# Optimization experiments

Measured on AMD Instinct MI355X. Metric: run time of the kernel, lower is better.

Reference implementation:

```python
import jax, jax.numpy as jnp
import numpy as np

B, T, D = 4, 1024, 768
HW = 32            # H = W = sqrt(T)
DS = D // 16       # d_state = 48
CHUNK = 8          # items_each_chunk (must divide W)


def _ln(x, w, b, eps=1e-5):
    mu = x.mean(-1, keepdims=True)
    var = ((x - mu) ** 2).mean(-1, keepdims=True)
    return (x - mu) / jnp.sqrt(var + eps) * w + b


def _conv1x1(x, w):  # x: (B,C,H,W), w: (O,C)
    return jnp.einsum('bchw,oc->bohw', x, w)


def _dwconv(x, w, b, pad):  # depthwise conv, w: (C,1,k,k)
    y = jax.lax.conv_general_dilated(
        x, w, (1, 1), [(pad, pad), (pad, pad)],
        dimension_numbers=('NCHW', 'OIHW', 'NCHW'),
        feature_group_count=x.shape[1])
    if b is not None:
        y = y + b[None, :, None, None]
    return y


def _norm_gates(Gl, Gm, Gr):
    gl, gm, gr = jax.nn.sigmoid(Gl), jax.nn.sigmoid(Gm), jax.nn.sigmoid(Gr)
    s = gl + gm + gr
    s = s.at[:, :, 0, :].set(gm[:, :, 0, :] + gr[:, :, 0, :])    # top row: no h-1 neighbor
    s = s.at[:, :, -1, :].set(gl[:, :, -1, :] + gm[:, :, -1, :])  # bottom row: no h+1 neighbor
    s = jnp.maximum(s, 1e-7)
    return gl / s, gm / s, gr / s


def _gspn_scan(X, L, Gl, Gm, Gr, chunk):
    # GateRecurrent2dnoind: scan along W in independent chunks of `chunk` columns.
    # H[:, :, h, t] = L*X + Gl*Hprev[h-1] + Gm*Hprev[h] + Gr*Hprev[h+1], Hprev=0 at chunk start.
    b, c, h, w = X.shape
    nc = w // chunk

    def to_scan(a):  # (B,C,H,W) -> (chunk, B, C, H, nc)
        return a.reshape(b, c, h, nc, chunk).transpose(4, 0, 1, 2, 3)

    xs, ls, gls, gms, grs = map(to_scan, (X, L, Gl, Gm, Gr))

    def step(hprev, inp):
        x, l, gl, gm, gr = inp
        h_up = jnp.pad(hprev[:, :, :-1], ((0, 0), (0, 0), (1, 0), (0, 0)))
        h_dn = jnp.pad(hprev[:, :, 1:], ((0, 0), (0, 0), (0, 1), (0, 0)))
        hn = l * x + gl * h_up + gm * hprev + gr * h_dn
        return hn, hn

    _, ys = jax.lax.scan(step, jnp.zeros((b, c, h, nc), X.dtype), (xs, ls, gls, gms, grs))
    return ys.transpose(1, 2, 3, 4, 0).reshape(b, c, h, w)


def setup_inputs() -> dict:
    key = jax.random.key(0)
    ks = jax.random.split(key, 16)
    s = 0.02
    return {
        'hidden_states': jax.random.normal(ks[0], (B, T, D), jnp.float32),
        'norm_w': jnp.ones((D,), jnp.float32),
        'norm_b': jnp.zeros((D,), jnp.float32),
        'in_proj_w': jax.random.normal(ks[1], (D, D), jnp.float32) * s,
        'conv7_w': jax.random.normal(ks[2], (D, 1, 7, 7), jnp.float32) * s,
        'conv7_b': jnp.zeros((D,), jnp.float32),
        'xdown_w': jax.random.normal(ks[3], (DS, D), jnp.float32) * s,
        'wup_w': jax.random.normal(ks[4], (12 * D, DS), jnp.float32) * s,
        'lup_w': jax.random.normal(ks[5], (4 * D, DS), jnp.float32) * s,
        'uup_w': jax.random.normal(ks[6], (4 * D, DS), jnp.float32) * s,
        'dcoef_w': jax.random.normal(ks[7], (4 * D, DS), jnp.float32) * s,
        'm_w': jax.random.normal(ks[8], (4,), jnp.float32) * 0.25,
        'outconv_w': jax.random.normal(ks[9], (D, D), jnp.float32) * s,
        'outdconv_w': jax.random.normal(ks[10], (D, 1, 3, 3), jnp.float32) * s,
        'outproj_w': jax.random.normal(ks[11], (D, D), jnp.float32) * s,
    }


def reference(hidden_states, norm_w, norm_b, in_proj_w, conv7_w, conv7_b,
              xdown_w, wup_w, lup_w, uup_w, dcoef_w, m_w,
              outconv_w, outdconv_w, outproj_w):
    b, t, d = hidden_states.shape
    hh = ww = HW
    shortcut = hidden_states
    x = _ln(shortcut, norm_w, norm_b)                      # (B,T,D)
    x = x.transpose(0, 2, 1).reshape(b, d, hh, ww)         # (B,D,H,W)
    x = _conv1x1(x, in_proj_w)
    x = _dwconv(x, conv7_w, conv7_b, 3)
    xp = _conv1x1(x, xdown_w)                              # (B,ds,H,W)
    ws = _conv1x1(xp, wup_w)                               # (B,12D,H,W)
    Ls = _conv1x1(xp, lup_w)                               # (B,4D,H,W)
    Us = _conv1x1(xp, uup_w)
    Ds = _conv1x1(xp, dcoef_w)
    # 4 scan directions: [x, x^T, flip_w(x), flip_w(x^T)]
    x_hwwh = jnp.stack([x, x.transpose(0, 1, 3, 2)], axis=1)       # (B,2,D,H,W)
    xs = jnp.concatenate([x_hwwh, x_hwwh[..., ::-1]], axis=1)      # (B,4,D,H,W)
    xs = xs.reshape(b, 4 * d, hh, ww)
    Gl, Gm, Gr = ws[:, :4 * d], ws[:, 4 * d:8 * d], ws[:, 8 * d:]
    gl, gm, gr = _norm_gates(Gl, Gm, Gr)
    out = _gspn_scan(xs, Ls, gl, gm, gr, CHUNK)
    out = out * Us + xs * Ds
    out = out.reshape(b, 4, d, hh, ww)
    out = jnp.einsum('bkdhw,k->bdhw', out, m_w)            # m_conv (1x1 over 4 dirs)
    out = _conv1x1(out, outconv_w)
    out = _dwconv(out, outdconv_w, None, 1)
    out = out * jax.nn.relu(out)
    out = out.reshape(b, d, t).transpose(0, 2, 1)
    out = out @ outproj_w.T
    return out, shortcut
```

## Files before the change

### kernel.cpp

```cpp
#include <hip/hip_runtime.h>

typedef unsigned short u16;
typedef unsigned int u32;
typedef __attribute__((ext_vector_type(8))) short short8v;
typedef __attribute__((ext_vector_type(4))) float f32x4;
typedef __attribute__((ext_vector_type(2))) unsigned u32x2v;

#define DD 768
#define PP 1024
#define NTOK 4096

__device__ __forceinline__ u16 f2bf(float f) {
  u32 u = __builtin_bit_cast(u32, f);
  u += 0x7fffu + ((u >> 16) & 1u);
  return (u16)(u >> 16);
}
__device__ __forceinline__ float b2f(u16 v) {
  return __builtin_bit_cast(float, (u32)v << 16);
}
__device__ __forceinline__ u32 pk_trunc(float fa, float fb) {
  return __builtin_amdgcn_perm(__builtin_bit_cast(u32, fa), __builtin_bit_cast(u32, fb), 0x07060302u);
}
__device__ __forceinline__ float ex8(const short8v& v, int j) {
  const u32 dw = ((const u32*)&v)[j >> 1];
  return __builtin_bit_cast(float, (j & 1) ? (dw & 0xffff0000u) : (dw << 16));
}
__device__ __forceinline__ float dpp_shr1(float x) {
  return __builtin_bit_cast(float,
      __builtin_amdgcn_update_dpp(0, __builtin_bit_cast(int, x), 0x138, 0xf, 0xf, true));
}
__device__ __forceinline__ float dpp_shl1(float x) {
  return __builtin_bit_cast(float,
      __builtin_amdgcn_update_dpp(0, __builtin_bit_cast(int, x), 0x130, 0xf, 0xf, true));
}
__device__ __forceinline__ float xhalf_sum(float p) {
#if __has_builtin(__builtin_amdgcn_permlane32_swap)
  u32x2v sw = __builtin_amdgcn_permlane32_swap(__builtin_bit_cast(u32, p),
                                               __builtin_bit_cast(u32, p), false, false);
  return __builtin_bit_cast(float, sw[0]) + __builtin_bit_cast(float, sw[1]);
#else
  return p + __shfl_xor(p, 32, 64);
#endif
}

__global__ __launch_bounds__(256) void prep_ln_k(const float* __restrict__ hs,
                                                 const float* __restrict__ gw, const float* __restrict__ gb,
                                                 u16* __restrict__ lnout, float* __restrict__ shortcut,
                                                 const float* __restrict__ win, u16* __restrict__ wInB,
                                                 const float* __restrict__ wout, u16* __restrict__ wOutB,
                                                 const float* __restrict__ wprj, u16* __restrict__ wPrjB,
                                                 const float* __restrict__ xdw, u16* __restrict__ wXdB,
                                                 const float* __restrict__ wup, const float* __restrict__ lup,
                                                 const float* __restrict__ uup, const float* __restrict__ dco,
                                                 u16* __restrict__ wB) {
  const int id = blockIdx.x;
  const int t = threadIdx.x;
  if (id < 4096) {
    const int tok = id;
    const float* xr = hs + (size_t)tok * DD;
    float v0 = xr[t], v1 = xr[t + 256], v2 = xr[t + 512];
    float s = v0 + v1 + v2;
    float q = v0 * v0 + v1 * v1 + v2 * v2;
#pragma unroll
    for (int off = 32; off > 0; off >>= 1) {
      s += __shfl_down(s, off, 64);
      q += __shfl_down(q, off, 64);
    }
    __shared__ float ss[4], qs[4];
    const int wid = t >> 6, lane = t & 63;
    if (lane == 0) { ss[wid] = s; qs[wid] = q; }
    __syncthreads();
    const float st = ss[0] + ss[1] + ss[2] + ss[3];
    const float qt = qs[0] + qs[1] + qs[2] + qs[3];
    const float mu = st * (1.f / 768.f);
    const float var = qt * (1.f / 768.f) - mu * mu;
    const float rstd = rsqrtf(var + 1e-5f);
    float* sc = shortcut + (size_t)tok * DD;
    u16* lo = lnout + (size_t)tok * DD;
    sc[t] = v0; sc[t + 256] = v1; sc[t + 512] = v2;
    lo[t]       = f2bf((v0 - mu) * rstd * gw[t] + gb[t]);
    lo[t + 256] = f2bf((v1 - mu) * rstd * gw[t + 256] + gb[t + 256]);
    lo[t + 512] = f2bf((v2 - mu) * rstd * gw[t + 512] + gb[t + 512]);
    return;
  }
  const int id2 = id - 4096;
  if (id2 < 6912) {
    const int m = id2 / 2304;
    const int i = (id2 - m * 2304) * 256 + t;
    const float* s = (m == 0) ? win : (m == 1) ? wout : wprj;
    u16* d = (m == 0) ? wInB : (m == 1) ? wOutB : wPrjB;
    d[i] = f2bf(s[i]);
  } else if (id2 < 7104) {
    const int i = (id2 - 6912) * 256 + t;
    const int r = i / DD;
    wXdB[i] = (r < 48) ? f2bf(xdw[i]) : (u16)0;
  } else {
    const int c = id2 - 7104;
    u16* dst = wB + (size_t)c * 2048;
    for (int i = t; i < 2048; i += 256) {
      const int row = i >> 6, s = i & 63;
      u16 v = 0;
      if (row < 24 && s < 48) {
        const int k = row & 3, type = row >> 2;
        const int ch = k * DD + c;
        const float* src;
        if (type < 3) src = wup + ((size_t)(type * 3072 + ch)) * 48;
        else if (type == 3) src = lup + (size_t)ch * 48;
        else if (type == 4) src = uup + (size_t)ch * 48;
        else src = dco + (size_t)ch * 48;
        v = f2bf(src[s]);
      }
      dst[i] = v;
    }
  }
}

template <int BSRC>
__global__ __launch_bounds__(256) void gemm_bf16(const u16* __restrict__ A,
                                                 const u16* __restrict__ Bt,
                                                 void* __restrict__ outv, const int mode) {
  __shared__ u16 Al[64][72];
  __shared__ u16 BlF[144 * 72];
  const int t = threadIdx.x;
  const int ntile = blockIdx.x * 128;
  const int mtile = blockIdx.y * 64;
  const int bb = ntile >> 10, pq0 = ntile & 1023;
  const int wid = t >> 6, lane = t & 63;
  const int m0 = (wid & 1) * 32, n0 = (wid >> 1) * 64;
  const int l15 = lane & 15, quad = lane >> 4;
  f32x4 acc[2][4];
#pragma unroll
  for (int mi = 0; mi < 2; ++mi)
#pragma unroll
    for (int ni = 0; ni < 4; ++ni) acc[mi][ni] = (f32x4){0.f, 0.f, 0.f, 0.f};
  const int ra = t >> 2, sa = t & 3;
  const u16* ag = A + (size_t)(mtile + ra) * DD + sa * 16;
  const int rb = t >> 1, hb = t & 1;
  const u16* bg = Bt + (size_t)(ntile + rb) * DD + hb * 32;
  const int chp = t >> 4, tok0 = (t & 15) * 8;
  const u16* bgc0 = Bt + ((size_t)(bb * DD + chp * 2)) * PP + pq0 + tok0;
  const u16* bgc1 = Bt + ((size_t)(bb * DD + (chp + 16) * 2)) * PP + pq0 + tok0;
  uint4 pa0, pa1, pb0, pb1, pb2, pb3;
#define LOADK(k0)                                                              \
  {                                                                            \
    pa0 = *reinterpret_cast<const uint4*>(ag + (k0));                          \
    pa1 = *reinterpret_cast<const uint4*>(ag + (k0) + 8);                      \
    if (BSRC == 0) {                                                           \
      pb0 = *reinterpret_cast<const uint4*>(bg + (k0));                        \
      pb1 = *reinterpret_cast<const uint4*>(bg + (k0) + 8);                    \
      pb2 = *reinterpret_cast<const uint4*>(bg + (k0) + 16);                   \
      pb3 = *reinterpret_cast<const uint4*>(bg + (k0) + 24);                   \
    } else {                                                                   \
      pb0 = *reinterpret_cast<const uint4*>(bgc0 + (size_t)(k0) * PP);         \
      pb1 = *reinterpret_cast<const uint4*>(bgc0 + (size_t)((k0) + 1) * PP);   \
      pb2 = *reinterpret_cast<const uint4*>(bgc1 + (size_t)(k0) * PP);         \
      pb3 = *reinterpret_cast<const uint4*>(bgc1 + (size_t)((k0) + 1) * PP);   \
    }                                                                          \
  }
  LOADK(0);
  for (int k0 = 0; k0 < DD; k0 += 64) {
    __syncthreads();
    *reinterpret_cast<uint4*>(&Al[ra][sa * 16]) = pa0;
    *reinterpret_cast<uint4*>(&Al[ra][sa * 16 + 8]) = pa1;
    if (BSRC == 0) {
      const int pr = rb + (rb >> 3);
      *reinterpret_cast<uint4*>(&BlF[pr * 72 + hb * 32]) = pb0;
      *reinterpret_cast<uint4*>(&BlF[pr * 72 + hb * 32 + 8]) = pb1;
      *reinterpret_cast<uint4*>(&BlF[pr * 72 + hb * 32 + 16]) = pb2;
      *reinterpret_cast<uint4*>(&BlF[pr * 72 + hb * 32 + 24]) = pb3;
    } else {
      union { uint4 v; u16 u[8]; } ua, ub, uc, ud;
      ua.v = pb0; ub.v = pb1; uc.v = pb2; ud.v = pb3;
#pragma unroll
      for (int i2 = 0; i2 < 8; ++i2) {
        const int prow = (tok0 + i2 + ((tok0 + i2) >> 3)) * 72;
        *reinterpret_cast<u32*>(&BlF[prow + chp * 2]) =
            (u32)ua.u[i2] | ((u32)ub.u[i2] << 16);
        *reinterpret_cast<u32*>(&BlF[prow + chp * 2 + 32]) =
            (u32)uc.u[i2] | ((u32)ud.u[i2] << 16);
      }
    }
    __syncthreads();
    if (k0 + 64 < DD) LOADK(k0 + 64);
    short8v af[2][2], bfr[4][2];
#pragma unroll
    for (int mi = 0; mi < 2; ++mi)
#pragma unroll
      for (int ks = 0; ks < 2; ++ks)
        af[mi][ks] = *reinterpret_cast<const short8v*>(&Al[m0 + mi * 16 + l15][ks * 32 + quad * 8]);
#pragma unroll
    for (int ni = 0; ni < 4; ++ni) {
      const int tl = n0 + ni * 16 + l15;
      const int prow = (tl + (tl >> 3)) * 72;
#pragma unroll
      for (int ks = 0; ks < 2; ++ks)
        bfr[ni][ks] = *reinterpret_cast<const short8v*>(&BlF[prow + ks * 32 + quad * 8]);
    }
#pragma unroll
    for (int mi = 0; mi < 2; ++mi)
#pragma unroll
      for (int ni = 0; ni < 4; ++ni) {
        acc[mi][ni] = __builtin_amdgcn_mfma_f32_16x16x32_bf16(af[mi][0], bfr[ni][0], acc[mi][ni], 0, 0, 0);
        acc[mi][ni] = __builtin_amdgcn_mfma_f32_16x16x32_bf16(af[mi][1], bfr[ni][1], acc[mi][ni], 0, 0, 0);
      }
  }
#undef LOADK
#pragma unroll
  for (int mi = 0; mi < 2; ++mi) {
#pragma unroll
    for (int ni = 0; ni < 4; ++ni) {
      const int ob = mtile + m0 + mi * 16 + quad * 4;
      const int pg = ntile + n0 + ni * 16 + l15;
      if (mode == 1) {
        *reinterpret_cast<f32x4*>((float*)outv + (size_t)pg * DD + ob) = acc[mi][ni];
      } else {
        const int pq = pg & 1023;
        u16* dstb = (u16*)outv;
#pragma unroll
        for (int r = 0; r < 4; ++r)
          dstb[((size_t)(bb * DD + ob + r)) * PP + pq] = f2bf(acc[mi][ni][r]);
      }
    }
  }
}

__global__ __launch_bounds__(256) void xdgemm_k(const u16* __restrict__ A,
                                                const u16* __restrict__ Ycm,
                                                u16* __restrict__ xpA) {
  __shared__ u16 Al[64][72];
  __shared__ u16 Bl[16][72];
  const int t = threadIdx.x;
  const int ntile = blockIdx.x * 16;
  const int bb = ntile >> 10, pq0 = ntile & 1023;
  const int wid = t >> 6, lane = t & 63, l15 = lane & 15, quad = lane >> 4;
  f32x4 acc = (f32x4){0.f, 0.f, 0.f, 0.f};
  const int arow = t >> 2, aks = (t & 3) * 16;
  const u16* ag = A + (size_t)arow * DD + aks;
  const int chp = t >> 3;
  const int tk0 = (t & 7) * 2;
  const u16* bg0 = Ycm + ((size_t)(bb * DD + chp * 2)) * PP + pq0 + tk0;
  for (int k0 = 0; k0 < DD; k0 += 64) {
    const uint4 a0 = *reinterpret_cast<const uint4*>(ag + k0);
    const uint4 a1 = *reinterpret_cast<const uint4*>(ag + k0 + 8);
    const u32 b0 = *reinterpret_cast<const u32*>(bg0 + (size_t)k0 * PP);
    const u32 b1 = *reinterpret_cast<const u32*>(bg0 + (size_t)(k0 + 1) * PP);
    __syncthreads();
    *reinterpret_cast<uint4*>(&Al[arow][aks]) = a0;
    *reinterpret_cast<uint4*>(&Al[arow][aks + 8]) = a1;
    *reinterpret_cast<u32*>(&Bl[tk0][chp * 2]) = (b0 & 0xffffu) | (b1 << 16);
    *reinterpret_cast<u32*>(&Bl[tk0 + 1][chp * 2]) = (b0 >> 16) | (b1 & 0xffff0000u);
    __syncthreads();
#pragma unroll
    for (int ks = 0; ks < 2; ++ks) {
      const short8v af = *reinterpret_cast<const short8v*>(&Al[wid * 16 + l15][ks * 32 + quad * 8]);
      const short8v bf = *reinterpret_cast<const short8v*>(&Bl[l15][ks * 32 + quad * 8]);
      acc = __builtin_amdgcn_mfma_f32_16x16x32_bf16(af, bf, acc, 0, 0, 0);
    }
  }
  const int pq = pq0 + l15;
  const int i = ((pq & 31) >> 4) * 512 + (pq >> 5) * 16 + (pq & 15);
  u16* dst = xpA + ((size_t)(bb * 1024 + i)) * 64 + wid * 16 + quad * 4;
  *reinterpret_cast<uint2*>(dst) = make_uint2(pk_trunc(acc[1], acc[0]), pk_trunc(acc[3], acc[2]));
}

__global__ __launch_bounds__(256) void dwconv7_k(const u16* __restrict__ x,
                                                 const float* __restrict__ wgt,
                                                 const float* __restrict__ bias,
                                                 u16* __restrict__ y) {
  const int bc = blockIdx.x;
  const int c = bc % DD;
  __shared__ float tile[38 * 38];
  __shared__ float wl[49];
  __shared__ float bsh[1];
  const int t = threadIdx.x;
  for (int i = t; i < 38 * 38; i += 256) tile[i] = 0.f;
  __syncthreads();
  const u16* xr = x + (size_t)bc * PP;
  for (int i = t; i < 512; i += 256) {
    const u32 v = reinterpret_cast<const u32*>(xr)[i];
    const int p0 = i * 2;
    const int h = p0 >> 5, w = p0 & 31;
    tile[(h + 3) * 38 + w + 3] = b2f((u16)v);
    tile[(h + 3) * 38 + w + 4] = b2f((u16)(v >> 16));
  }
  if (t < 49) wl[t] = wgt[c * 49 + t];
  if (t == 0) bsh[0] = bias[c];
  __syncthreads();
  u16* yo = y + (size_t)bc * PP;
  const int w = t & 31, hb = t >> 5;
  const float bv = bsh[0];
  float a0 = bv, a1 = bv, a2 = bv, a3 = bv;
#pragma unroll
  for (int rr = 0; rr < 10; ++rr) {
    float row[7];
#pragma unroll
    for (int kw = 0; kw < 7; ++kw) row[kw] = tile[(hb * 4 + rr) * 38 + w + kw];
    if (rr < 7) {
#pragma unroll
      for (int kw = 0; kw < 7; ++kw) a0 = fmaf(wl[rr * 7 + kw], row[kw], a0);
    }
    if (rr >= 1 && rr < 8) {
#pragma unroll
      for (int kw = 0; kw < 7; ++kw) a1 = fmaf(wl[(rr - 1) * 7 + kw], row[kw], a1);
    }
    if (rr >= 2 && rr < 9) {
#pragma unroll
      for (int kw = 0; kw < 7; ++kw) a2 = fmaf(wl[(rr - 2) * 7 + kw], row[kw], a2);
    }
    if (rr >= 3) {
#pragma unroll
      for (int kw = 0; kw < 7; ++kw) a3 = fmaf(wl[(rr - 3) * 7 + kw], row[kw], a3);
    }
  }
  yo[(hb * 4 + 0) * 32 + w] = f2bf(a0);
  yo[(hb * 4 + 1) * 32 + w] = f2bf(a1);
  yo[(hb * 4 + 2) * 32 + w] = f2bf(a2);
  yo[(hb * 4 + 3) * 32 + w] = f2bf(a3);
}

__global__ __launch_bounds__(256) void dwconv3_k(const u16* __restrict__ x,
                                                 const float* __restrict__ wgt,
                                                 u16* __restrict__ y) {
  const int bc = blockIdx.x;
  const int c = bc % DD;
  __shared__ float tile[34 * 34];
  __shared__ float wl[9];
  const int t = threadIdx.x;
  for (int i = t; i < 34 * 34; i += 256) tile[i] = 0.f;
  __syncthreads();
  const u16* xr = x + (size_t)bc * PP;
  for (int i = t; i < 512; i += 256) {
    const u32 v = reinterpret_cast<const u32*>(xr)[i];
    const int p0 = i * 2;
    const int h = p0 >> 5, w = p0 & 31;
    tile[(h + 1) * 34 + w + 1] = b2f((u16)v);
    tile[(h + 1) * 34 + w + 2] = b2f((u16)(v >> 16));
  }
  if (t < 9) wl[t] = wgt[c * 9 + t];
  __syncthreads();
  u16* yo = y + (size_t)bc * PP;
  const int w = t & 31, hb = t >> 5;
  float a0 = 0.f, a1 = 0.f, a2 = 0.f, a3 = 0.f;
#pragma unroll
  for (int rr = 0; rr < 6; ++rr) {
    float row[3];
#pragma unroll
    for (int kw = 0; kw < 3; ++kw) row[kw] = tile[(hb * 4 + rr) * 34 + w + kw];
    if (rr < 3) {
#pragma unroll
      for (int kw = 0; kw < 3; ++kw) a0 = fmaf(wl[rr * 3 + kw], row[kw], a0);
    }
    if (rr >= 1 && rr < 4) {
#pragma unroll
      for (int kw = 0; kw < 3; ++kw) a1 = fmaf(wl[(rr - 1) * 3 + kw], row[kw], a1);
    }
    if (rr >= 2 && rr < 5) {
#pragma unroll
      for (int kw = 0; kw < 3; ++kw) a2 = fmaf(wl[(rr - 2) * 3 + kw], row[kw], a2);
    }
    if (rr >= 3) {
#pragma unroll
      for (int kw = 0; kw < 3; ++kw) a3 = fmaf(wl[(rr - 3) * 3 + kw], row[kw], a3);
    }
  }
  const float r0 = a0 > 0.f ? a0 * a0 : 0.f;
  const float r1 = a1 > 0.f ? a1 * a1 : 0.f;
  const float r2 = a2 > 0.f ? a2 * a2 : 0.f;
  const float r3 = a3 > 0.f ? a3 * a3 : 0.f;
  yo[(hb * 4 + 0) * 32 + w] = f2bf(r0);
  yo[(hb * 4 + 1) * 32 + w] = f2bf(r1);
  yo[(hb * 4 + 2) * 32 + w] = f2bf(r2);
  yo[(hb * 4 + 3) * 32 + w] = f2bf(r3);
}

#define ACT_SWZ(row, col) ((col) ^ (((((col) >> 6) ^ (row)) & 7) << 3))
#define PSWZ(r) ((((r) ^ ((r) >> 3)) & 3) << 3)

__device__ __forceinline__ void produce_half(u16* __restrict__ actbuf,
                                             const u16* __restrict__ ab,
                                             const short8v bw[2][2],
                                             int l15, int quad, int g) {
#pragma unroll
  for (int mt = 0; mt < 8; ++mt) {
    const u16* ar = ab + (mt * 16 + l15) * 64 + quad * 8;
    const short8v a0 = *reinterpret_cast<const short8v*>(ar);
    const short8v a1 = *reinterpret_cast<const short8v*>(ar + 32);
    f32x4 acc0 = {0.f, 0.f, 0.f, 0.f}, acc1 = {0.f, 0.f, 0.f, 0.f};
    acc0 = __builtin_amdgcn_mfma_f32_16x16x32_bf16(a0, bw[0][0], acc0, 0, 0, 0);
    acc0 = __builtin_amdgcn_mfma_f32_16x16x32_bf16(a1, bw[0][1], acc0, 0, 0, 0);
    acc1 = __builtin_amdgcn_mfma_f32_16x16x32_bf16(a0, bw[1][0], acc1, 0, 0, 0);
    acc1 = __builtin_amdgcn_mfma_f32_16x16x32_bf16(a1, bw[1][1], acc1, 0, 0, 0);
    const int qb = g * 128 + mt * 16 + quad * 4;
    const int cs = ACT_SWZ(l15, qb);
    *reinterpret_cast<uint2*>(&actbuf[l15 * 512 + cs]) =
        make_uint2(pk_trunc(acc0[1], acc0[0]), pk_trunc(acc0[3], acc0[2]));
    if (l15 < 8)
      *reinterpret_cast<uint2*>(&actbuf[(16 + l15) * 512 + cs]) =
          make_uint2(pk_trunc(acc1[1], acc1[0]), pk_trunc(acc1[3], acc1[2]));
  }
}

__device__ __forceinline__ void consume_half(const u16* __restrict__ actbuf,
                                             const u16* __restrict__ planeTc,
                                             const u16* __restrict__ y2row,
                                             u16* __restrict__ outpc,
                                             float mw, int dpair, int cs2, int d, int h, int half) {
  __builtin_amdgcn_s_setprio(1);
  const int k = dpair * 2 + d;
  const int hc = half * 2 + cs2;
  const int colb = h * 16 + cs2 * 8;
  const int wst = dpair ? (24 - hc * 8) : (hc * 8);
  short8v vPr;
  if (d == 0) vPr = *reinterpret_cast<const short8v*>(y2row + h * 32 + wst);
  else        vPr = *reinterpret_cast<const short8v*>(planeTc + h * 40 + (wst ^ PSWZ(h)));
  short8v vPe;
  {
    const u32* s = (const u32*)&vPr;
    u32* dq = (u32*)&vPe;
    if (dpair) {
      dq[0] = (s[3] >> 16) | (s[3] << 16);
      dq[1] = (s[2] >> 16) | (s[2] << 16);
      dq[2] = (s[1] >> 16) | (s[1] << 16);
      dq[3] = (s[0] >> 16) | (s[0] << 16);
    } else {
      dq[0] = s[0]; dq[1] = s[1]; dq[2] = s[2]; dq[3] = s[3];
    }
  }
#define ACTP(row) (*reinterpret_cast<const short8v*>(&actbuf[(row) * 512 + ACT_SWZ((row), colb)]))
  const short8v vGl = ACTP(0 + k);
  const short8v vGm = ACTP(4 + k);
  const short8v vGr = ACTP(8 + k);
  const short8v vL  = ACTP(12 + k);
  const short8v vU  = ACTP(16 + k);
  const short8v vD  = ACTP(20 + k);
#undef ACTP
  const bool top = (h == 0), bot = (h == 31);
  float H = 0.f, prev = 0.f;
  u32 ox[4];
#pragma unroll
  for (int j = 0; j < 8; ++j) {
    float el = __expf(-ex8(vGl, j));
    const float em = __expf(-ex8(vGm, j));
    float er = __expf(-ex8(vGr, j));
    if (top) el = 1e30f;
    if (bot) er = 1e30f;
    const float pl2 = 1.f + el, pm = 1.f + em, pr = 1.f + er;
    const float ul = pm * pr, um = pl2 * pr, ur = pl2 * pm;
    const float rcpS = __builtin_amdgcn_rcpf(ul + um + ur);
    const float xv = ex8(vPe, j);
    const float Lx = ex8(vL, j) * xv;
    const float up = dpp_shr1(H);
    const float dn = dpp_shl1(H);
    H = fmaf(ul * rcpS, up, fmaf(um * rcpS, H, fmaf(ur * rcpS, dn, Lx)));
    float part = fmaf(H, ex8(vU, j), xv * ex8(vD, j)) * mw;
    part = xhalf_sum(part);
    if (j & 1) ox[j >> 1] = pk_trunc(part, prev);
    else prev = part;
  }
  if (d == 0) {
    uint4 o;
    o.x = ox[0]; o.y = ox[1]; o.z = ox[2]; o.w = ox[3];
    *reinterpret_cast<uint4*>(&outpc[h * 64 + dpair * 32 + ((hc * 8) ^ ((h & 3) << 3))]) = o;
  }
  __builtin_amdgcn_s_setprio(0);
}

__global__ __launch_bounds__(512, 4) void scan_k(const u16* __restrict__ y2b,
                                                 const u16* __restrict__ xpA,
                                                 const u16* __restrict__ wB,
                                                 const float* __restrict__ mwp,
                                                 u16* __restrict__ out1) {
  const int bc2 = blockIdx.x;
  const int b = bc2 / 384;
  const int cpair = bc2 - b * 384;
  const int c0 = cpair * 2;
  __shared__ __align__(16) u16 actA[24 * 512];
  __shared__ __align__(16) u16 actB[24 * 512];
  __shared__ __align__(16) u16 planeT[2][1280];
  __shared__ __align__(16) u16 outp[2][32 * 64];
  const int t = threadIdx.x;
  const int wid = t >> 6, lane = t & 63, l15 = lane & 15, quad = lane >> 4;
  const int ch = wid >> 2;
  const int g = wid & 3;
  const int dpair = g & 1, cs2 = g >> 1;
  const int d = lane >> 5, h = lane & 31;
  const int c = c0 + ch;
  const int bc = b * DD + c;
  {
    const int pch = t >> 8, idx = t & 255;
    const u16* yp = y2b + (size_t)(b * DD + c0 + pch) * PP;
#pragma unroll
    for (int i2 = 0; i2 < 2; ++i2) {
      const int i = idx + i2 * 256;
      const u32 v = reinterpret_cast<const u32*>(yp)[i];
      const int p0 = i * 2;
      const int hh = p0 >> 5, ww = p0 & 31;
      planeT[pch][ww * 40 + (hh ^ PSWZ(ww))] = (u16)v;
      planeT[pch][(ww + 1) * 40 + (hh ^ PSWZ(ww + 1))] = (u16)(v >> 16);
    }
  }
  const u16* wc = wB + (size_t)c * 2048;
  short8v bw[2][2];
#pragma unroll
  for (int nt = 0; nt < 2; ++nt)
#pragma unroll
    for (int ks = 0; ks < 2; ++ks)
      bw[nt][ks] = *reinterpret_cast<const short8v*>(wc + (nt * 16 + l15) * 64 + ks * 32 + quad * 8);
  const u16* xb = xpA + ((size_t)(b * 1024)) * 64;
  const u16* y2row = y2b + (size_t)bc * PP;
  const float mw = mwp[dpair * 2 + d];
  if (ch == 0) produce_half(actA, xb + (size_t)(g * 128) * 64, bw, l15, quad, g);
  __syncthreads();
  if (ch == 0) consume_half(actA, planeT[0], y2row, outp[0], mw, dpair, cs2, d, h, 0);
  else         produce_half(actB, xb + (size_t)(g * 128) * 64, bw, l15, quad, g);
  __syncthreads();
  if (ch == 1) consume_half(actB, planeT[1], y2row, outp[1], mw, dpair, cs2, d, h, 0);
  else         produce_half(actA, xb + (size_t)(512 + g * 128) * 64, bw, l15, quad, g);
  __syncthreads();
  if (ch == 0) consume_half(actA, planeT[0], y2row, outp[0], mw, dpair, cs2, d, h, 1);
  else         produce_half(actB, xb + (size_t)(512 + g * 128) * 64, bw, l15, quad, g);
  __syncthreads();
  if (ch == 1) consume_half(actB, planeT[1], y2row, outp[1], mw, dpair, cs2, d, h, 1);
  __syncthreads();
  const int hh2 = t >> 4, wp = t & 15;
  const int wsw = (wp * 2) ^ ((hh2 & 3) << 3);
#pragma unroll
  for (int cc = 0; cc < 2; ++cc) {
    const u32 u0 = *reinterpret_cast<const u32*>(&outp[cc][hh2 * 64 + wsw]);
    const u32 u1 = *reinterpret_cast<const u32*>(&outp[cc][hh2 * 64 + 32 + wsw]);
    const float v0 = b2f((u16)u0) + b2f((u16)u1);
    const float v1 = b2f((u16)(u0 >> 16)) + b2f((u16)(u1 >> 16));
    *reinterpret_cast<u32*>(out1 + (size_t)(b * DD + c0 + cc) * PP + hh2 * 32 + wp * 2) =
        pk_trunc(v1, v0);
  }
}

extern "C" void kernel_launch(void* const* d_in, const int* in_sizes, int n_in,
                              void* d_out, int out_size, void* d_ws, size_t ws_size,
                              hipStream_t stream) {
  const float* hs   = (const float*)d_in[0];
  const float* nw   = (const float*)d_in[1];
  const float* nb   = (const float*)d_in[2];
  const float* win  = (const float*)d_in[3];
  const float* c7w  = (const float*)d_in[4];
  const float* c7b  = (const float*)d_in[5];
  const float* xdw  = (const float*)d_in[6];
  const float* wupw = (const float*)d_in[7];
  const float* lupw = (const float*)d_in[8];
  const float* uupw = (const float*)d_in[9];
  const float* dcow = (const float*)d_in[10];
  const float* mww  = (const float*)d_in[11];
  const float* wout = (const float*)d_in[12];
  const float* odw  = (const float*)d_in[13];
  const float* wprj = (const float*)d_in[14];
  float* out0 = (float*)d_out;
  float* shortcut = out0 + (size_t)NTOK * DD;

  char* ws = (char*)d_ws;
  u16* lnA    = (u16*)(ws + 0);
  u16* wInB   = (u16*)(ws + 6291456);
  u16* wOutB  = (u16*)(ws + 7471104);
  u16* wPrjB  = (u16*)(ws + 8650752);
  u16* wB     = (u16*)(ws + 9830400);
  u16* wXdB   = (u16*)(ws + 12976128);
  u16* xpA    = (u16*)(ws + 13074432);
  u16* y1b    = (u16*)(ws + 13598720);
  u16* y2b    = (u16*)(ws + 19890176);
  u16* out1   = (u16*)(ws + 26181632);
  u16* y3b    = y1b;
  u16* y4b    = out1;

  prep_ln_k<<<11968, 256, 0, stream>>>(hs, nw, nb, lnA, shortcut,
                                       win, wInB, wout, wOutB, wprj, wPrjB,
                                       xdw, wXdB, wupw, lupw, uupw, dcow, wB);
  gemm_bf16<0><<<dim3(32, 12), 256, 0, stream>>>(wInB, lnA, y1b, 3);
  dwconv7_k<<<3072, 256, 0, stream>>>(y1b, c7w, c7b, y2b);
  xdgemm_k<<<256, 256, 0, stream>>>(wXdB, y2b, xpA);
  scan_k<<<1536, 512, 0, stream>>>(y2b, xpA, wB, mww, out1);
  gemm_bf16<1><<<dim3(32, 12), 256, 0, stream>>>(wOutB, out1, y3b, 3);
  dwconv3_k<<<3072, 256, 0, stream>>>(y3b, odw, y4b);
  gemm_bf16<1><<<dim3(32, 12), 256, 0, stream>>>(wPrjB, y4b, out0, 1);
}
```

Measured before the change: 226.5 us.

## Load GEMM operands directly into MFMA registers, bypassing shared memory

Replaces the templated shared-memory GEMM with two kernels. The first (in_proj) loads A and B fragments straight from global memory into MFMA register layout, with no LDS and no barriers, and double-buffers the even and odd k-halves. The second (out_conv/out_proj) still transposes B through LDS, but now packs four channels per 8-byte store and loads A fragments directly from global memory. The aim is to cut LDS traffic and synchronisation, at the cost of less coalesced global loads and more reliance on cache for operand reuse.

```diff
diff --git a/kernel.cpp b/kernel.cpp
--- a/kernel.cpp
+++ b/kernel.cpp
@@ -115,11 +115,92 @@
   }
 }
 
-template <int BSRC>
-__global__ __launch_bounds__(256) void gemm_bf16(const u16* __restrict__ A,
-                                                 const u16* __restrict__ Bt,
-                                                 void* __restrict__ outv, const int mode) {
-  __shared__ u16 Al[64][72];
+__global__ __launch_bounds__(256) void gemm_nl(const u16* __restrict__ A,
+                                               const u16* __restrict__ Bt,
+                                               void* __restrict__ outv, const int mode) {
+  const int t = threadIdx.x;
+  const int ntile = blockIdx.x * 128;
+  const int mtile = blockIdx.y * 64;
+  const int bb = ntile >> 10;
+  const int wid = t >> 6, lane = t & 63;
+  const int m0 = (wid & 1) * 32, n0 = (wid >> 1) * 64;
+  const int l15 = lane & 15, quad = lane >> 4;
+  f32x4 acc[2][4];
+#pragma unroll
+  for (int mi = 0; mi < 2; ++mi)
+#pragma unroll
+    for (int ni = 0; ni < 4; ++ni) acc[mi][ni] = (f32x4){0.f, 0.f, 0.f, 0.f};
+  const u16* a0p = A + (size_t)(mtile + m0 + l15) * DD + quad * 8;
+  const u16* a1p = a0p + (size_t)16 * DD;
+  const u16* b0p = Bt + (size_t)(ntile + n0 + l15) * DD + quad * 8;
+  const u16* b1p = b0p + (size_t)16 * DD;
+  const u16* b2p = b0p + (size_t)32 * DD;
+  const u16* b3p = b0p + (size_t)48 * DD;
+  short8v a0e, a1e, b0e, b1e, b2e, b3e;
+  short8v a0o, a1o, b0o, b1o, b2o, b3o;
+#define LOADE(k0)                                              \
+  {                                                            \
+    a0e = *reinterpret_cast<const short8v*>(a0p + (k0));       \
+    a1e = *reinterpret_cast<const short8v*>(a1p + (k0));       \
+    b0e = *reinterpret_cast<const short8v*>(b0p + (k0));       \
+    b1e = *reinterpret_cast<const short8v*>(b1p + (k0));       \
+    b2e = *reinterpret_cast<const short8v*>(b2p + (k0));       \
+    b3e = *reinterpret_cast<const short8v*>(b3p + (k0));       \
+  }
+#define LOADO(k0)                                              \
+  {                                                            \
+    a0o = *reinterpret_cast<const short8v*>(a0p + (k0));       \
+    a1o = *reinterpret_cast<const short8v*>(a1p + (k0));       \
+    b0o = *reinterpret_cast<const short8v*>(b0p + (k0));       \
+    b1o = *reinterpret_cast<const short8v*>(b1p + (k0));       \
+    b2o = *reinterpret_cast<const short8v*>(b2p + (k0));       \
+    b3o = *reinterpret_cast<const short8v*>(b3p + (k0));       \
+  }
+  LOADE(0);
+  for (int k0 = 0; k0 < DD; k0 += 64) {
+    LOADO(k0 + 32);
+    acc[0][0] = __builtin_amdgcn_mfma_f32_16x16x32_bf16(a0e, b0e, acc[0][0], 0, 0, 0);
+    acc[0][1] = __builtin_amdgcn_mfma_f32_16x16x32_bf16(a0e, b1e, acc[0][1], 0, 0, 0);
+    acc[0][2] = __builtin_amdgcn_mfma_f32_16x16x32_bf16(a0e, b2e, acc[0][2], 0, 0, 0);
+    acc[0][3] = __builtin_amdgcn_mfma_f32_16x16x32_bf16(a0e, b3e, acc[0][3], 0, 0, 0);
+    acc[1][0] = __builtin_amdgcn_mfma_f32_16x16x32_bf16(a1e, b0e, acc[1][0], 0, 0, 0);
+    acc[1][1] = __builtin_amdgcn_mfma_f32_16x16x32_bf16(a1e, b1e, acc[1][1], 0, 0, 0);
+    acc[1][2] = __builtin_amdgcn_mfma_f32_16x16x32_bf16(a1e, b2e, acc[1][2], 0, 0, 0);
+    acc[1][3] = __builtin_amdgcn_mfma_f32_16x16x32_bf16(a1e, b3e, acc[1][3], 0, 0, 0);
+    if (k0 + 64 < DD) LOADE(k0 + 64);
+    acc[0][0] = __builtin_amdgcn_mfma_f32_16x16x32_bf16(a0o, b0o, acc[0][0], 0, 0, 0);
+    acc[0][1] = __builtin_amdgcn_mfma_f32_16x16x32_bf16(a0o, b1o, acc[0][1], 0, 0, 0);
+    acc[0][2] = __builtin_amdgcn_mfma_f32_16x16x32_bf16(a0o, b2o, acc[0][2], 0, 0, 0);
+    acc[0][3] = __builtin_amdgcn_mfma_f32_16x16x32_bf16(a0o, b3o, acc[0][3], 0, 0, 0);
+    acc[1][0] = __builtin_amdgcn_mfma_f32_16x16x32_bf16(a1o, b0o, acc[1][0], 0, 0, 0);
+    acc[1][1] = __builtin_amdgcn_mfma_f32_16x16x32_bf16(a1o, b1o, acc[1][1], 0, 0, 0);
+    acc[1][2] = __builtin_amdgcn_mfma_f32_16x16x32_bf16(a1o, b2o, acc[1][2], 0, 0, 0);
+    acc[1][3] = __builtin_amdgcn_mfma_f32_16x16x32_bf16(a1o, b3o, acc[1][3], 0, 0, 0);
+  }
+#undef LOADE
+#undef LOADO
+#pragma unroll
+  for (int mi = 0; mi < 2; ++mi) {
+#pragma unroll
+    for (int ni = 0; ni < 4; ++ni) {
+      const int ob = mtile + m0 + mi * 16 + quad * 4;
+      const int pg = ntile + n0 + ni * 16 + l15;
+      if (mode == 1) {
+        *reinterpret_cast<f32x4*>((float*)outv + (size_t)pg * DD + ob) = acc[mi][ni];
+      } else {
+        const int pq = pg & 1023;
+        u16* dstb = (u16*)outv;
+#pragma unroll
+        for (int r = 0; r < 4; ++r)
+          dstb[((size_t)(bb * DD + ob + r)) * PP + pq] = f2bf(acc[mi][ni][r]);
+      }
+    }
+  }
+}
+
+__global__ __launch_bounds__(256) void gemm_cm(const u16* __restrict__ A,
+                                               const u16* __restrict__ Bt,
+                                               void* __restrict__ outv, const int mode) {
   __shared__ u16 BlF[144 * 72];
   const int t = threadIdx.x;
   const int ntile = blockIdx.x * 128;
@@ -133,61 +214,50 @@
   for (int mi = 0; mi < 2; ++mi)
 #pragma unroll
     for (int ni = 0; ni < 4; ++ni) acc[mi][ni] = (f32x4){0.f, 0.f, 0.f, 0.f};
-  const int ra = t >> 2, sa = t & 3;
-  const u16* ag = A + (size_t)(mtile + ra) * DD + sa * 16;
-  const int rb = t >> 1, hb = t & 1;
-  const u16* bg = Bt + (size_t)(ntile + rb) * DD + hb * 32;
   const int chp = t >> 4, tok0 = (t & 15) * 8;
-  const u16* bgc0 = Bt + ((size_t)(bb * DD + chp * 2)) * PP + pq0 + tok0;
-  const u16* bgc1 = Bt + ((size_t)(bb * DD + (chp + 16) * 2)) * PP + pq0 + tok0;
-  uint4 pa0, pa1, pb0, pb1, pb2, pb3;
-#define LOADK(k0)                                                              \
-  {                                                                            \
-    pa0 = *reinterpret_cast<const uint4*>(ag + (k0));                          \
-    pa1 = *reinterpret_cast<const uint4*>(ag + (k0) + 8);                      \
-    if (BSRC == 0) {                                                           \
-      pb0 = *reinterpret_cast<const uint4*>(bg + (k0));                        \
-      pb1 = *reinterpret_cast<const uint4*>(bg + (k0) + 8);                    \
-      pb2 = *reinterpret_cast<const uint4*>(bg + (k0) + 16);                   \
-      pb3 = *reinterpret_cast<const uint4*>(bg + (k0) + 24);                   \
-    } else {                                                                   \
-      pb0 = *reinterpret_cast<const uint4*>(bgc0 + (size_t)(k0) * PP);         \
-      pb1 = *reinterpret_cast<const uint4*>(bgc0 + (size_t)((k0) + 1) * PP);   \
-      pb2 = *reinterpret_cast<const uint4*>(bgc1 + (size_t)(k0) * PP);         \
-      pb3 = *reinterpret_cast<const uint4*>(bgc1 + (size_t)((k0) + 1) * PP);   \
-    }                                                                          \
-  }
-  LOADK(0);
+  const u16* bgc = Bt + ((size_t)(bb * DD + chp * 4)) * PP + pq0 + tok0;
+  const u16* a0p = A + (size_t)(mtile + m0 + l15) * DD + quad * 8;
+  const u16* a1p = a0p + (size_t)16 * DD;
+  uint4 pb0, pb1, pb2, pb3;
+  short8v paf[2][2];
+#define LOADB(k0)                                                            \
+  {                                                                          \
+    pb0 = *reinterpret_cast<const uint4*>(bgc + (size_t)(k0) * PP);          \
+    pb1 = *reinterpret_cast<const uint4*>(bgc + (size_t)((k0) + 1) * PP);    \
+    pb2 = *reinterpret_cast<const uint4*>(bgc + (size_t)((k0) + 2) * PP);    \
+    pb3 = *reinterpret_cast<const uint4*>(bgc + (size_t)((k0) + 3) * PP);    \
+  }
+#define LOADA(k0)                                                            \
+  {                                                                          \
+    paf[0][0] = *reinterpret_cast<const short8v*>(a0p + (k0));               \
+    paf[0][1] = *reinterpret_cast<const short8v*>(a0p + (k0) + 32);          \
+    paf[1][0] = *reinterpret_cast<const short8v*>(a1p + (k0));               \
+    paf[1][1] = *reinterpret_cast<const short8v*>(a1p + (k0) + 32);          \
+  }
+  LOADB(0);
+  LOADA(0);
   for (int k0 = 0; k0 < DD; k0 += 64) {
     __syncthreads();
-    *reinterpret_cast<uint4*>(&Al[ra][sa * 16]) = pa0;
-    *reinterpret_cast<uint4*>(&Al[ra][sa * 16 + 8]) = pa1;
-    if (BSRC == 0) {
-      const int pr = rb + (rb >> 3);
-      *reinterpret_cast<uint4*>(&BlF[pr * 72 + hb * 32]) = pb0;
-      *reinterpret_cast<uint4*>(&BlF[pr * 72 + hb * 32 + 8]) = pb1;
-      *reinterpret_cast<uint4*>(&BlF[pr * 72 + hb * 32 + 16]) = pb2;
-      *reinterpret_cast<uint4*>(&BlF[pr * 72 + hb * 32 + 24]) = pb3;
-    } else {
+    {
       union { uint4 v; u16 u[8]; } ua, ub, uc, ud;
       ua.v = pb0; ub.v = pb1; uc.v = pb2; ud.v = pb3;
 #pragma unroll
       for (int i2 = 0; i2 < 8; ++i2) {
-        const int prow = (tok0 + i2 + ((tok0 + i2) >> 3)) * 72;
-        *reinterpret_cast<u32*>(&BlF[prow + chp * 2]) =
-            (u32)ua.u[i2] | ((u32)ub.u[i2] << 16);
-        *reinterpret_cast<u32*>(&BlF[prow + chp * 2 + 32]) =
-            (u32)uc.u[i2] | ((u32)ud.u[i2] << 16);
+        const int tk = tok0 + i2;
+        const int prow = (tk + (tk >> 3)) * 72;
+        *reinterpret_cast<uint2*>(&BlF[prow + chp * 4]) =
+            make_uint2((u32)ua.u[i2] | ((u32)ub.u[i2] << 16),
+                       (u32)uc.u[i2] | ((u32)ud.u[i2] << 16));
       }
     }
     __syncthreads();
-    if (k0 + 64 < DD) LOADK(k0 + 64);
-    short8v af[2][2], bfr[4][2];
+    short8v af[2][2];
 #pragma unroll
     for (int mi = 0; mi < 2; ++mi)
 #pragma unroll
-      for (int ks = 0; ks < 2; ++ks)
-        af[mi][ks] = *reinterpret_cast<const short8v*>(&Al[m0 + mi * 16 + l15][ks * 32 + quad * 8]);
+      for (int ks = 0; ks < 2; ++ks) af[mi][ks] = paf[mi][ks];
+    if (k0 + 64 < DD) { LOADB(k0 + 64); LOADA(k0 + 64); }
+    short8v bfr[4][2];
 #pragma unroll
     for (int ni = 0; ni < 4; ++ni) {
       const int tl = n0 + ni * 16 + l15;
@@ -204,7 +274,8 @@
         acc[mi][ni] = __builtin_amdgcn_mfma_f32_16x16x32_bf16(af[mi][1], bfr[ni][1], acc[mi][ni], 0, 0, 0);
       }
   }
-#undef LOADK
+#undef LOADB
+#undef LOADA
 #pragma unroll
   for (int mi = 0; mi < 2; ++mi) {
 #pragma unroll
@@ -573,11 +644,11 @@
   prep_ln_k<<<11968, 256, 0, stream>>>(hs, nw, nb, lnA, shortcut,
                                        win, wInB, wout, wOutB, wprj, wPrjB,
                                        xdw, wXdB, wupw, lupw, uupw, dcow, wB);
-  gemm_bf16<0><<<dim3(32, 12), 256, 0, stream>>>(wInB, lnA, y1b, 3);
+  gemm_nl<<<dim3(32, 12), 256, 0, stream>>>(wInB, lnA, y1b, 3);
   dwconv7_k<<<3072, 256, 0, stream>>>(y1b, c7w, c7b, y2b);
   xdgemm_k<<<256, 256, 0, stream>>>(wXdB, y2b, xpA);
   scan_k<<<1536, 512, 0, stream>>>(y2b, xpA, wB, mww, out1);
-  gemm_bf16<1><<<dim3(32, 12), 256, 0, stream>>>(wOutB, out1, y3b, 3);
+  gemm_cm<<<dim3(32, 12), 256, 0, stream>>>(wOutB, out1, y3b, 3);
   dwconv3_k<<<3072, 256, 0, stream>>>(y3b, odw, y4b);
-  gemm_bf16<1><<<dim3(32, 12), 256, 0, stream>>>(wPrjB, y4b, out0, 1);
-}
+  gemm_cm<<<dim3(32, 12), 256, 0, stream>>>(wPrjB, y4b, out0, 1);
+}
```

After: 252.3 us. 1.11x slower.
